# Optimization experiments

Measured on AMD Instinct MI355X. Metric: run time of the kernel, lower is better.

Reference implementation:

```python
import jax, jax.numpy as jnp
import numpy as np

N_HEADS = 16
QUANT_BITS = 8


def fake_quantize(x, bits=QUANT_BITS):
    # Global max-abs fake quantization with STE (grad = identity).
    if bits >= 16:
        return x
    max_val = jnp.max(jnp.abs(x))
    half_levels = jnp.asarray(2.0 ** (bits - 1), x.dtype)
    q = jnp.round(x / max_val * half_levels) / half_levels * max_val
    q = jnp.where(max_val > 0, q, x)
    return x + jax.lax.stop_gradient(q - x)


def qat_linear(x, W, b):
    # torch nn.Linear: y = x @ W.T + b, with fake-quant on input and output.
    xq = fake_quantize(x)
    y = jnp.einsum('bsd,od->bso', xq, W) + b
    return fake_quantize(y)


def setup_inputs() -> dict:
    key = jax.random.key(0)
    ks = jax.random.split(key, 9)
    d = 1024
    B, S = 2, 2048
    scale = 1.0 / np.sqrt(d)
    return {
        'x': jax.random.normal(ks[0], (B, S, d), jnp.float32),
        'Wq': jax.random.normal(ks[1], (d, d), jnp.float32) * scale,
        'bq': jax.random.normal(ks[2], (d,), jnp.float32) * 0.01,
        'Wk': jax.random.normal(ks[3], (d, d), jnp.float32) * scale,
        'bk': jax.random.normal(ks[4], (d,), jnp.float32) * 0.01,
        'Wv': jax.random.normal(ks[5], (d, d), jnp.float32) * scale,
        'bv': jax.random.normal(ks[6], (d,), jnp.float32) * 0.01,
        'Wo': jax.random.normal(ks[7], (d, d), jnp.float32) * scale,
        'bo': jax.random.normal(ks[8], (d,), jnp.float32) * 0.01,
    }


def reference(x, Wq, bq, Wk, bk, Wv, bv, Wo, bo):
    B, S, d_model = x.shape
    d_k = d_model // N_HEADS

    def split_heads(t):  # [B,S,D] -> [B,H,S,dk]
        return t.reshape(B, S, N_HEADS, d_k).transpose(0, 2, 1, 3)

    Q = split_heads(qat_linear(x, Wq, bq))
    K = split_heads(qat_linear(x, Wk, bk))
    V = split_heads(qat_linear(x, Wv, bv))

    scores = jnp.einsum('bhqd,bhkd->bhqk', Q, K) / jnp.sqrt(jnp.asarray(d_k, x.dtype))
    attn = jax.nn.softmax(scores, axis=-1)  # dropout = identity (deterministic ref)
    out = jnp.einsum('bhqk,bhkd->bhqd', attn, V)
    out = out.transpose(0, 2, 1, 3).reshape(B, S, d_model)
    return qat_linear(out, Wo, bo)
```

## Files before the change

kernel.cpp:

```cpp
#include <hip/hip_runtime.h>
#include <math.h>

#define DMODEL 1024
#define SEQ    2048
#define NELEM  4194304
#define N4     (NELEM / 4)

typedef __attribute__((ext_vector_type(8))) short short8;
typedef __attribute__((ext_vector_type(4))) short short4v;
typedef __attribute__((ext_vector_type(4))) float f32x4;

#if __has_builtin(__builtin_amdgcn_exp2f)
#define EXP2(x) __builtin_amdgcn_exp2f(x)
#else
#define EXP2(x) exp2f(x)
#endif

__device__ __forceinline__ void gl2lds16(const unsigned short* g, unsigned short* l) {
    __builtin_amdgcn_global_load_lds(
        (const __attribute__((address_space(1))) unsigned int*)g,
        (__attribute__((address_space(3))) unsigned int*)l,
        16, 0, 0);
}

__device__ __forceinline__ float fq(float x, float m) {
    float t = x / m * 128.0f;
    float r = rintf(t);
    float q = r * 0.0078125f * m;
    return (m > 0.0f) ? q : x;
}
__device__ __forceinline__ unsigned short f2bf(float f) {
    unsigned int u = __float_as_uint(f);
    u += 0x7FFFu + ((u >> 16) & 1u);
    return (unsigned short)(u >> 16);
}
__device__ __forceinline__ float bf2f(unsigned short h) {
    return __uint_as_float(((unsigned int)h) << 16);
}
__device__ __forceinline__ unsigned short qint(float x, float m) {
    float i = rintf(x / m * 128.0f);
    return (unsigned short)(__float_as_uint(i) >> 16);
}

__device__ __forceinline__ void block_max_atomic(float v, float* red, unsigned int* slot) {
    const int t = threadIdx.x;
    red[t] = v;
    __syncthreads();
    #pragma unroll
    for (int s = 128; s > 0; s >>= 1) {
        if (t < s) red[t] = fmaxf(red[t], red[t + s]);
        __syncthreads();
    }
    if (t == 0) atomicMax(slot, __float_as_uint(red[0]));
}

__global__ __launch_bounds__(256) void absmax_kernel(const float* __restrict__ x, int n4,
                                                     unsigned int* __restrict__ slot) {
    __shared__ float red[256];
    float m = 0.0f;
    const float4* x4 = (const float4*)x;
    for (int i = blockIdx.x * 256 + threadIdx.x; i < n4; i += gridDim.x * 256) {
        float4 v = x4[i];
        m = fmaxf(m, fmaxf(fmaxf(fabsf(v.x), fabsf(v.y)), fmaxf(fabsf(v.z), fabsf(v.w))));
    }
    block_max_atomic(m, red, slot);
}

__global__ __launch_bounds__(256) void quant_int_kernel(const float* __restrict__ src,
                                                        unsigned short* __restrict__ dst,
                                                        const unsigned int* __restrict__ slot,
                                                        int n4) {
    const float m = __uint_as_float(*slot);
    const float4* s4 = (const float4*)src;
    for (int i = blockIdx.x * 256 + threadIdx.x; i < n4; i += gridDim.x * 256) {
        float4 v = s4[i];
        ushort4 o;
        o.x = qint(v.x, m); o.y = qint(v.y, m); o.z = qint(v.z, m); o.w = qint(v.w, m);
        ((ushort4*)dst)[i] = o;
    }
}

__global__ __launch_bounds__(256) void quant_out_kernel(float* __restrict__ Y,
                                                        const unsigned int* __restrict__ slot,
                                                        int n4) {
    const float m = __uint_as_float(*slot);
    float4* y4 = (float4*)Y;
    for (int i = blockIdx.x * 256 + threadIdx.x; i < n4; i += gridDim.x * 256) {
        float4 v = y4[i];
        v.x = fq(v.x, m); v.y = fq(v.y, m); v.z = fq(v.z, m); v.w = fq(v.w, m);
        y4[i] = v;
    }
}

__global__ __launch_bounds__(256) void wsplit_kernel(
    const float* __restrict__ W0, const float* __restrict__ W1,
    const float* __restrict__ W2, const float* __restrict__ W3,
    unsigned short* __restrict__ H0, unsigned short* __restrict__ L0,
    unsigned short* __restrict__ H1, unsigned short* __restrict__ L1,
    unsigned short* __restrict__ H2, unsigned short* __restrict__ L2,
    unsigned short* __restrict__ H3, unsigned short* __restrict__ L3) {
    const int z = blockIdx.y;
    const float* W = (z == 0) ? W0 : (z == 1) ? W1 : (z == 2) ? W2 : W3;
    unsigned short* H = (z == 0) ? H0 : (z == 1) ? H1 : (z == 2) ? H2 : H3;
    unsigned short* L = (z == 0) ? L0 : (z == 1) ? L1 : (z == 2) ? L2 : L3;
    const int i = blockIdx.x * 256 + threadIdx.x;
    float4 w = ((const float4*)W)[i];
    ushort4 h, l;
    h.x = f2bf(w.x); l.x = f2bf(w.x - bf2f(h.x));
    h.y = f2bf(w.y); l.y = f2bf(w.y - bf2f(h.y));
    h.z = f2bf(w.z); l.z = f2bf(w.z - bf2f(h.z));
    h.w = f2bf(w.w); l.w = f2bf(w.w - bf2f(h.w));
    ((ushort4*)H)[i] = h;
    ((ushort4*)L)[i] = l;
}

__global__ __launch_bounds__(256) void vtrans_quant(const float* __restrict__ Vraw,
                                                    unsigned short* __restrict__ Vti,
                                                    const unsigned int* __restrict__ slot) {
    __shared__ float tile[64][65];
    const float mv = __uint_as_float(*slot);
    const int t = threadIdx.x;
    const int s0 = blockIdx.x << 6;
    const int bh = blockIdx.y;
    const int b = bh >> 4, h = bh & 15;
    const int rr = t >> 4;
    const int cc = (t & 15) << 2;
    #pragma unroll
    for (int rep = 0; rep < 4; rep++) {
        int srow = rep * 16 + rr;
        float4 v = *(const float4*)&Vraw[(size_t)b * SEQ * DMODEL + (size_t)(s0 + srow) * DMODEL + h * 64 + cc];
        tile[srow][cc + 0] = v.x; tile[srow][cc + 1] = v.y;
        tile[srow][cc + 2] = v.z; tile[srow][cc + 3] = v.w;
    }
    __syncthreads();
    #pragma unroll
    for (int rep = 0; rep < 4; rep++) {
        int drow = rep * 16 + rr;
        ushort4 o;
        o.x = qint(tile[cc + 0][drow], mv);
        o.y = qint(tile[cc + 1][drow], mv);
        o.z = qint(tile[cc + 2][drow], mv);
        o.w = qint(tile[cc + 3][drow], mv);
        *(ushort4*)&Vti[(size_t)bh * 64 * SEQ + (size_t)drow * SEQ + s0 + cc] = o;
    }
}

template<int BN>
__global__ __launch_bounds__(256) void gemm_mfma(
    const unsigned short* __restrict__ Ai, const unsigned int* __restrict__ mSlot,
    const unsigned short* __restrict__ Wh0, const unsigned short* __restrict__ Wl0,
    const float* __restrict__ b0, float* __restrict__ O0, unsigned int* __restrict__ s0,
    const unsigned short* __restrict__ Wh1, const unsigned short* __restrict__ Wl1,
    const float* __restrict__ b1, float* __restrict__ O1, unsigned int* __restrict__ s1) {
    constexpr int NI = BN / 32;
    __shared__ __align__(16) unsigned short As[128 * 32];
    __shared__ __align__(16) unsigned short Bh[BN * 32];
    __shared__ __align__(16) unsigned short Bl[BN * 32];
    __shared__ float red[256];

    const int z = blockIdx.z;
    const unsigned short* Wh = z ? Wh1 : Wh0;
    const unsigned short* Wl = z ? Wl1 : Wl0;
    const float* bias = z ? b1 : b0;
    float* O = z ? O1 : O0;
    unsigned int* slotOut = z ? s1 : s0;

    const float mA = __uint_as_float(*mSlot);
    const int t = threadIdx.x;
    const int lane = t & 63, w = t >> 6;
    const int ml = lane & 15, qd = lane >> 4;
    const int wm = w & 1, wn = w >> 1;
    const int m0 = blockIdx.y << 7;
    const int n0 = blockIdx.x * BN;

    const int lr = lane >> 2;
    const int lc = (lane & 3) << 3;
    const unsigned short* Asrc = Ai + (size_t)(m0 + w * 32 + lr) * DMODEL + lc;
    const unsigned short* Hsrc = Wh + (size_t)(n0 + w * (BN / 4) + lr) * DMODEL + lc;
    const unsigned short* Lsrc = Wl + (size_t)(n0 + w * (BN / 4) + lr) * DMODEL + lc;
    unsigned short* Adst = &As[(w * 32) * 32];
    unsigned short* Hdst = &Bh[(w * (BN / 4)) * 32];
    unsigned short* Ldst = &Bl[(w * (BN / 4)) * 32];

    f32x4 acc[4][NI];
    #pragma unroll
    for (int mi = 0; mi < 4; mi++)
        #pragma unroll
        for (int ni = 0; ni < NI; ni++) acc[mi][ni] = (f32x4){0.f, 0.f, 0.f, 0.f};

    for (int k0 = 0; k0 < DMODEL; k0 += 32) {
        __syncthreads();
        gl2lds16(Asrc + k0,               Adst);
        gl2lds16(Asrc + k0 + 16 * DMODEL, Adst + 16 * 32);
        if constexpr (BN == 128) {
            gl2lds16(Hsrc + k0,               Hdst);
            gl2lds16(Hsrc + k0 + 16 * DMODEL, Hdst + 16 * 32);
            gl2lds16(Lsrc + k0,               Ldst);
            gl2lds16(Lsrc + k0 + 16 * DMODEL, Ldst + 16 * 32);
        } else {
            gl2lds16(Hsrc + k0, Hdst);
            gl2lds16(Lsrc + k0, Ldst);
        }
        __syncthreads();

        short8 af[4];
        #pragma unroll
        for (int mi = 0; mi < 4; mi++)
            af[mi] = *(const short8*)&As[(wm * 64 + mi * 16 + ml) * 32 + qd * 8];
        #pragma unroll
        for (int ni = 0; ni < NI; ni++) {
            short8 bh = *(const short8*)&Bh[(wn * (BN / 2) + ni * 16 + ml) * 32 + qd * 8];
            short8 bl = *(const short8*)&Bl[(wn * (BN / 2) + ni * 16 + ml) * 32 + qd * 8];
            #pragma unroll
            for (int mi = 0; mi < 4; mi++) {
                acc[mi][ni] = __builtin_amdgcn_mfma_f32_16x16x32_bf16(af[mi], bh, acc[mi][ni], 0, 0, 0);
                acc[mi][ni] = __builtin_amdgcn_mfma_f32_16x16x32_bf16(af[mi], bl, acc[mi][ni], 0, 0, 0);
            }
        }
    }

    const float s = mA * 0.0078125f;
    float lmax = 0.0f;
    #pragma unroll
    for (int ni = 0; ni < NI; ni++) {
        const int col = n0 + wn * (BN / 2) + ni * 16 + ml;
        const float bc = bias[col];
        #pragma unroll
        for (int mi = 0; mi < 4; mi++) {
            #pragma unroll
            for (int r = 0; r < 4; r++) {
                int row = m0 + wm * 64 + mi * 16 + qd * 4 + r;
                float v = acc[mi][ni][r] * s + bc;
                lmax = fmaxf(lmax, fabsf(v));
                O[row * DMODEL + col] = v;
            }
        }
    }
    block_max_atomic(lmax, red, slotOut);
}

__global__ __launch_bounds__(256) void attn_mfma(
    const float* __restrict__ Qraw, const unsigned short* __restrict__ Ki,
    const unsigned short* __restrict__ Vti, const unsigned int* __restrict__ slots,
    float* __restrict__ Out, unsigned int* __restrict__ moSlot) {
    __shared__ __align__(16) unsigned short Ks[64 * 72];
    __shared__ __align__(16) unsigned short Vt[64 * 72];
    __shared__ float red[256];
    union U8 { short8 v; unsigned short u[8]; };
    union U4 { short4v v; unsigned short u[4]; };

    const int t = threadIdx.x;
    const int lane = t & 63, w = t >> 6;
    const int ml = lane & 15, qd = lane >> 4;
    const int q0 = blockIdx.x << 6;
    const int bh = blockIdx.y;
    const int b = bh >> 4, h = bh & 15;
    const float mq = __uint_as_float(slots[1]);
    const float mk = __uint_as_float(slots[2]);
    const float mv = __uint_as_float(slots[3]);
    const float c2 = (mq * 0.0078125f) * (mk * 0.0078125f) * 0.125f * 1.4426950408889634f;
    const int baseQ = b * SEQ * DMODEL + h * 64;
    const int qg = q0 + w * 16 + ml;

    short8 bq[2];
    {
        const float* src = Qraw + baseQ + qg * DMODEL + qd * 8;
        #pragma unroll
        for (int c = 0; c < 2; c++) {
            float4 v0 = *(const float4*)(src + c * 32);
            float4 v1 = *(const float4*)(src + c * 32 + 4);
            U8 tmp;
            tmp.u[0] = qint(v0.x, mq); tmp.u[1] = qint(v0.y, mq);
            tmp.u[2] = qint(v0.z, mq); tmp.u[3] = qint(v0.w, mq);
            tmp.u[4] = qint(v1.x, mq); tmp.u[5] = qint(v1.y, mq);
            tmp.u[6] = qint(v1.z, mq); tmp.u[7] = qint(v1.w, mq);
            bq[c] = tmp.v;
        }
    }

    f32x4 oacc[4];
    #pragma unroll
    for (int i = 0; i < 4; i++) oacc[i] = (f32x4){0.f, 0.f, 0.f, 0.f};
    float mrun = -INFINITY, lrun = 0.0f;

    const int sr = t >> 2;
    const int sc = (t & 3) << 4;
    const unsigned short* kstage = Ki + baseQ + (size_t)sr * DMODEL + sc;
    const unsigned short* vstage = Vti + (size_t)bh * 64 * SEQ + (size_t)sr * SEQ + sc;

    for (int k0 = 0; k0 < SEQ; k0 += 64) {
        __syncthreads();
        *(short8*)&Ks[sr * 72 + sc]     = *(const short8*)(kstage + (size_t)k0 * DMODEL);
        *(short8*)&Ks[sr * 72 + sc + 8] = *(const short8*)(kstage + (size_t)k0 * DMODEL + 8);
        *(short8*)&Vt[sr * 72 + sc]     = *(const short8*)(vstage + k0);
        *(short8*)&Vt[sr * 72 + sc + 8] = *(const short8*)(vstage + k0 + 8);
        __syncthreads();

        f32x4 sacc[4];
        #pragma unroll
        for (int tau = 0; tau < 4; tau++) {
            short8 a0 = *(const short8*)&Ks[(tau * 16 + ml) * 72 + qd * 8];
            short8 a1 = *(const short8*)&Ks[(tau * 16 + ml) * 72 + 32 + qd * 8];
            f32x4 z4 = (f32x4){0.f, 0.f, 0.f, 0.f};
            z4 = __builtin_amdgcn_mfma_f32_16x16x32_bf16(a0, bq[0], z4, 0, 0, 0);
            sacc[tau] = __builtin_amdgcn_mfma_f32_16x16x32_bf16(a1, bq[1], z4, 0, 0, 0);
        }

        float tmax = fmaxf(fmaxf(fmaxf(sacc[0][0], sacc[0][1]), fmaxf(sacc[0][2], sacc[0][3])),
                           fmaxf(fmaxf(sacc[1][0], sacc[1][1]), fmaxf(sacc[1][2], sacc[1][3])));
        tmax = fmaxf(tmax, fmaxf(fmaxf(fmaxf(sacc[2][0], sacc[2][1]), fmaxf(sacc[2][2], sacc[2][3])),
                                 fmaxf(fmaxf(sacc[3][0], sacc[3][1]), fmaxf(sacc[3][2], sacc[3][3]))));
        tmax = fmaxf(tmax, __shfl_xor(tmax, 16));
        tmax = fmaxf(tmax, __shfl_xor(tmax, 32));
        const float mnew = fmaxf(mrun, tmax);
        const float alpha = EXP2((mrun - mnew) * c2);
        const float mc = mnew * c2;
        float p[4][4];
        float ls = 0.0f;
        #pragma unroll
        for (int tau = 0; tau < 4; tau++)
            #pragma unroll
            for (int r = 0; r < 4; r++) {
                float pv = EXP2(sacc[tau][r] * c2 - mc);
                p[tau][r] = pv;
                ls += pv;
            }
        ls += __shfl_xor(ls, 16);
        ls += __shfl_xor(ls, 32);
        lrun = lrun * alpha + ls;
        mrun = mnew;

        short4v phi[4], plo[4];
        #pragma unroll
        for (int tau = 0; tau < 4; tau++) {
            U4 hh, ll;
            #pragma unroll
            for (int r = 0; r < 4; r++) {
                unsigned int u = __float_as_uint(p[tau][r]);
                unsigned int uh = (u + 0x8000u) & 0xFFFF0000u;
                hh.u[r] = (unsigned short)(uh >> 16);
                float lf = p[tau][r] - __uint_as_float(uh);
                ll.u[r] = (unsigned short)(__float_as_uint(lf) >> 16);
            }
            phi[tau] = hh.v;
            plo[tau] = ll.v;
        }

        #pragma unroll
        for (int i = 0; i < 4; i++) {
            oacc[i][0] *= alpha; oacc[i][1] *= alpha;
            oacc[i][2] *= alpha; oacc[i][3] *= alpha;
        }

        #pragma unroll
        for (int td = 0; td < 4; td++) {
            #pragma unroll
            for (int tau = 0; tau < 4; tau++) {
                short4v av = *(const short4v*)&Vt[(td * 16 + ml) * 72 + tau * 16 + qd * 4];
                oacc[td] = __builtin_amdgcn_mfma_f32_16x16x16bf16_1k(av, phi[tau], oacc[td], 0, 0, 0);
                oacc[td] = __builtin_amdgcn_mfma_f32_16x16x16bf16_1k(av, plo[tau], oacc[td], 0, 0, 0);
            }
        }
    }

    const float inv = (mv * 0.0078125f) / lrun;
    float lmax = 0.0f;
    #pragma unroll
    for (int td = 0; td < 4; td++) {
        float4 o;
        o.x = oacc[td][0] * inv;
        o.y = oacc[td][1] * inv;
        o.z = oacc[td][2] * inv;
        o.w = oacc[td][3] * inv;
        lmax = fmaxf(lmax, fmaxf(fmaxf(fabsf(o.x), fabsf(o.y)), fmaxf(fabsf(o.z), fabsf(o.w))));
        *(float4*)&Out[baseQ + (size_t)qg * DMODEL + td * 16 + qd * 4] = o;
    }
    block_max_atomic(lmax, red, moSlot);
}

extern "C" void kernel_launch(void* const* d_in, const int* in_sizes, int n_in,
                              void* d_out, int out_size, void* d_ws, size_t ws_size,
                              hipStream_t stream) {
    const float* x  = (const float*)d_in[0];
    const float* Wq = (const float*)d_in[1];
    const float* bq = (const float*)d_in[2];
    const float* Wk = (const float*)d_in[3];
    const float* bk = (const float*)d_in[4];
    const float* Wv = (const float*)d_in[5];
    const float* bv = (const float*)d_in[6];
    const float* Wo = (const float*)d_in[7];
    const float* bo = (const float*)d_in[8];
    float* out = (float*)d_out;

    const size_t MB = 1024 * 1024;
    unsigned int* slots = (unsigned int*)d_ws;
    char* p = (char*)d_ws + 256;
    unsigned short* WqH = (unsigned short*)(p + 0 * MB);
    unsigned short* WqL = (unsigned short*)(p + 2 * MB);
    unsigned short* WkH = (unsigned short*)(p + 4 * MB);
    unsigned short* WkL = (unsigned short*)(p + 6 * MB);
    unsigned short* WvH = (unsigned short*)(p + 8 * MB);
    unsigned short* WvL = (unsigned short*)(p + 10 * MB);
    unsigned short* WoH = (unsigned short*)(p + 12 * MB);
    unsigned short* WoL = (unsigned short*)(p + 14 * MB);
    unsigned short* Xi  = (unsigned short*)(p + 16 * MB);
    float* RA  = (float*)(p + 24 * MB);
    float* RB  = (float*)(p + 40 * MB);
    unsigned short* Vti = (unsigned short*)(p + 56 * MB);
    unsigned short* Ki  = (unsigned short*)(p + 4 * MB);
    unsigned short* Oi  = (unsigned short*)RA;

    hipMemsetAsync(d_ws, 0, 256, stream);

    wsplit_kernel<<<dim3(1024, 4), 256, 0, stream>>>(Wq, Wk, Wv, Wo,
        WqH, WqL, WkH, WkL, WvH, WvL, WoH, WoL);
    absmax_kernel<<<1024, 256, 0, stream>>>(x, N4, slots + 0);
    quant_int_kernel<<<1024, 256, 0, stream>>>(x, Xi, slots + 0, N4);

    gemm_mfma<128><<<dim3(8, 32, 2), 256, 0, stream>>>(Xi, slots + 0,
        WkH, WkL, bk, RA, slots + 2,
        WvH, WvL, bv, RB, slots + 3);
    quant_int_kernel<<<1024, 256, 0, stream>>>(RA, Ki, slots + 2, N4);
    vtrans_quant<<<dim3(32, 32), 256, 0, stream>>>(RB, Vti, slots + 3);

    gemm_mfma<64><<<dim3(16, 32, 1), 256, 0, stream>>>(Xi, slots + 0,
        WqH, WqL, bq, RA, slots + 1,
        WqH, WqL, bq, RA, slots + 1);

    attn_mfma<<<dim3(32, 32), 256, 0, stream>>>(RA, Ki, Vti, slots, RB, slots + 4);
    quant_int_kernel<<<1024, 256, 0, stream>>>(RB, Oi, slots + 4, N4);

    gemm_mfma<64><<<dim3(16, 32, 1), 256, 0, stream>>>(Oi, slots + 4,
        WoH, WoL, bo, out, slots + 5,
        WoH, WoL, bo, out, slots + 5);
    quant_out_kernel<<<1024, 256, 0, stream>>>(out, slots + 5, N4);
}
```

Measured before the change: 341.1 us.

## Fuse Q projection into KV GEMM launch and double-buffer attention K/V tiles

The Q projection now runs in the same launch as the K and V projections as a third z-slice, using the BN=128 tile config and writing raw Q into the output buffer as scratch. This removes one kernel launch and gives a larger grid. The attention kernel double-buffers its K/V LDS tiles: the next tile is prefetched into registers during compute and written to the alternate buffer, so each iteration needs one barrier instead of two. In exchange, LDS use and register pressure go up, which could lower occupancy.

```diff
diff --git a/kernel.cpp b/kernel.cpp
--- a/kernel.cpp
+++ b/kernel.cpp
@@ -151,7 +151,9 @@
     const unsigned short* __restrict__ Wh0, const unsigned short* __restrict__ Wl0,
     const float* __restrict__ b0, float* __restrict__ O0, unsigned int* __restrict__ s0,
     const unsigned short* __restrict__ Wh1, const unsigned short* __restrict__ Wl1,
-    const float* __restrict__ b1, float* __restrict__ O1, unsigned int* __restrict__ s1) {
+    const float* __restrict__ b1, float* __restrict__ O1, unsigned int* __restrict__ s1,
+    const unsigned short* __restrict__ Wh2, const unsigned short* __restrict__ Wl2,
+    const float* __restrict__ b2, float* __restrict__ O2, unsigned int* __restrict__ s2) {
     constexpr int NI = BN / 32;
     __shared__ __align__(16) unsigned short As[128 * 32];
     __shared__ __align__(16) unsigned short Bh[BN * 32];
@@ -159,11 +161,11 @@
     __shared__ float red[256];
 
     const int z = blockIdx.z;
-    const unsigned short* Wh = z ? Wh1 : Wh0;
-    const unsigned short* Wl = z ? Wl1 : Wl0;
-    const float* bias = z ? b1 : b0;
-    float* O = z ? O1 : O0;
-    unsigned int* slotOut = z ? s1 : s0;
+    const unsigned short* Wh = (z == 0) ? Wh0 : (z == 1) ? Wh1 : Wh2;
+    const unsigned short* Wl = (z == 0) ? Wl0 : (z == 1) ? Wl1 : Wl2;
+    const float* bias = (z == 0) ? b0 : (z == 1) ? b1 : b2;
+    float* O = (z == 0) ? O0 : (z == 1) ? O1 : O2;
+    unsigned int* slotOut = (z == 0) ? s0 : (z == 1) ? s1 : s2;
 
     const float mA = __uint_as_float(*mSlot);
     const int t = threadIdx.x;
@@ -243,8 +245,8 @@
     const float* __restrict__ Qraw, const unsigned short* __restrict__ Ki,
     const unsigned short* __restrict__ Vti, const unsigned int* __restrict__ slots,
     float* __restrict__ Out, unsigned int* __restrict__ moSlot) {
-    __shared__ __align__(16) unsigned short Ks[64 * 72];
-    __shared__ __align__(16) unsigned short Vt[64 * 72];
+    __shared__ __align__(16) unsigned short Ks[2][64 * 72];
+    __shared__ __align__(16) unsigned short Vt[2][64 * 72];
     __shared__ float red[256];
     union U8 { short8 v; unsigned short u[8]; };
     union U4 { short4v v; unsigned short u[4]; };
@@ -288,19 +290,34 @@
     const unsigned short* kstage = Ki + baseQ + (size_t)sr * DMODEL + sc;
     const unsigned short* vstage = Vti + (size_t)bh * 64 * SEQ + (size_t)sr * SEQ + sc;
 
-    for (int k0 = 0; k0 < SEQ; k0 += 64) {
-        __syncthreads();
-        *(short8*)&Ks[sr * 72 + sc]     = *(const short8*)(kstage + (size_t)k0 * DMODEL);
-        *(short8*)&Ks[sr * 72 + sc + 8] = *(const short8*)(kstage + (size_t)k0 * DMODEL + 8);
-        *(short8*)&Vt[sr * 72 + sc]     = *(const short8*)(vstage + k0);
-        *(short8*)&Vt[sr * 72 + sc + 8] = *(const short8*)(vstage + k0 + 8);
-        __syncthreads();
+    {
+        short8 a = *(const short8*)kstage;
+        short8 bb = *(const short8*)(kstage + 8);
+        short8 c = *(const short8*)vstage;
+        short8 d = *(const short8*)(vstage + 8);
+        *(short8*)&Ks[0][sr * 72 + sc] = a;
+        *(short8*)&Ks[0][sr * 72 + sc + 8] = bb;
+        *(short8*)&Vt[0][sr * 72 + sc] = c;
+        *(short8*)&Vt[0][sr * 72 + sc + 8] = d;
+    }
+    __syncthreads();
+
+    for (int it = 0; it < 32; it++) {
+        const int cur = it & 1;
+        short8 nk0, nk1, nv0, nv1;
+        if (it < 31) {
+            const size_t ko = (size_t)(it + 1) * 64;
+            nk0 = *(const short8*)(kstage + ko * DMODEL);
+            nk1 = *(const short8*)(kstage + ko * DMODEL + 8);
+            nv0 = *(const short8*)(vstage + ko);
+            nv1 = *(const short8*)(vstage + ko + 8);
+        }
 
         f32x4 sacc[4];
         #pragma unroll
         for (int tau = 0; tau < 4; tau++) {
-            short8 a0 = *(const short8*)&Ks[(tau * 16 + ml) * 72 + qd * 8];
-            short8 a1 = *(const short8*)&Ks[(tau * 16 + ml) * 72 + 32 + qd * 8];
+            short8 a0 = *(const short8*)&Ks[cur][(tau * 16 + ml) * 72 + qd * 8];
+            short8 a1 = *(const short8*)&Ks[cur][(tau * 16 + ml) * 72 + 32 + qd * 8];
             f32x4 z4 = (f32x4){0.f, 0.f, 0.f, 0.f};
             z4 = __builtin_amdgcn_mfma_f32_16x16x32_bf16(a0, bq[0], z4, 0, 0, 0);
             sacc[tau] = __builtin_amdgcn_mfma_f32_16x16x32_bf16(a1, bq[1], z4, 0, 0, 0);
@@ -356,11 +373,19 @@
         for (int td = 0; td < 4; td++) {
             #pragma unroll
             for (int tau = 0; tau < 4; tau++) {
-                short4v av = *(const short4v*)&Vt[(td * 16 + ml) * 72 + tau * 16 + qd * 4];
+                short4v av = *(const short4v*)&Vt[cur][(td * 16 + ml) * 72 + tau * 16 + qd * 4];
                 oacc[td] = __builtin_amdgcn_mfma_f32_16x16x16bf16_1k(av, phi[tau], oacc[td], 0, 0, 0);
                 oacc[td] = __builtin_amdgcn_mfma_f32_16x16x16bf16_1k(av, plo[tau], oacc[td], 0, 0, 0);
             }
         }
+
+        if (it < 31) {
+            *(short8*)&Ks[cur ^ 1][sr * 72 + sc] = nk0;
+            *(short8*)&Ks[cur ^ 1][sr * 72 + sc + 8] = nk1;
+            *(short8*)&Vt[cur ^ 1][sr * 72 + sc] = nv0;
+            *(short8*)&Vt[cur ^ 1][sr * 72 + sc + 8] = nv1;
+        }
+        __syncthreads();
     }
 
     const float inv = (mv * 0.0078125f) / lrun;
@@ -409,6 +434,7 @@
     unsigned short* Vti = (unsigned short*)(p + 56 * MB);
     unsigned short* Ki  = (unsigned short*)(p + 4 * MB);
     unsigned short* Oi  = (unsigned short*)RA;
+    float* Qraw = out;
 
     hipMemsetAsync(d_ws, 0, 256, stream);
 
@@ -417,20 +443,18 @@
     absmax_kernel<<<1024, 256, 0, stream>>>(x, N4, slots + 0);
     quant_int_kernel<<<1024, 256, 0, stream>>>(x, Xi, slots + 0, N4);
 
-    gemm_mfma<128><<<dim3(8, 32, 2), 256, 0, stream>>>(Xi, slots + 0,
-        WkH, WkL, bk, RA, slots + 2,
-        WvH, WvL, bv, RB, slots + 3);
+    gemm_mfma<128><<<dim3(8, 32, 3), 256, 0, stream>>>(Xi, slots + 0,
+        WqH, WqL, bq, Qraw, slots + 1,
+        WkH, WkL, bk, RA,   slots + 2,
+        WvH, WvL, bv, RB,   slots + 3);
     quant_int_kernel<<<1024, 256, 0, stream>>>(RA, Ki, slots + 2, N4);
     vtrans_quant<<<dim3(32, 32), 256, 0, stream>>>(RB, Vti, slots + 3);
 
-    gemm_mfma<64><<<dim3(16, 32, 1), 256, 0, stream>>>(Xi, slots + 0,
-        WqH, WqL, bq, RA, slots + 1,
-        WqH, WqL, bq, RA, slots + 1);
-
-    attn_mfma<<<dim3(32, 32), 256, 0, stream>>>(RA, Ki, Vti, slots, RB, slots + 4);
+    attn_mfma<<<dim3(32, 32), 256, 0, stream>>>(Qraw, Ki, Vti, slots, RB, slots + 4);
     quant_int_kernel<<<1024, 256, 0, stream>>>(RB, Oi, slots + 4, N4);
 
     gemm_mfma<64><<<dim3(16, 32, 1), 256, 0, stream>>>(Oi, slots + 4,
+        WoH, WoL, bo, out, slots + 5,
         WoH, WoL, bo, out, slots + 5,
         WoH, WoL, bo, out, slots + 5);
     quant_out_kernel<<<1024, 256, 0, stream>>>(out, slots + 5, N4);
```

Result: faster. 331.2 us (-2.9%).
